# Kernel optimization log

Hardware: AMD Instinct MI355X
Metric: run time of the kernel (lower is better)

Reference implementation:

```python
import jax, jax.numpy as jnp
import numpy as np

D_MODEL = 1024
D_PROJ = D_MODEL // 4


def setup_inputs() -> dict:
    key = jax.random.key(0)
    k1, k2, k3 = jax.random.split(key, 3)
    hidden_states = jax.random.normal(k1, (4, 2048, D_MODEL), dtype=jnp.float32)
    proj_w = jax.random.normal(k2, (D_PROJ, D_MODEL), dtype=jnp.float32) * 0.02
    proj_b = jnp.zeros((D_PROJ,), dtype=jnp.float32)
    clf_w = jax.random.normal(k3, (1, 1), dtype=jnp.float32) * 0.02
    clf_b = jnp.zeros((1,), dtype=jnp.float32)
    return {"hidden_states": hidden_states, "proj_w": proj_w, "proj_b": proj_b,
            "clf_w": clf_w, "clf_b": clf_b}


def reference(hidden_states, proj_w, proj_b, clf_w, clf_b):
    # h: [B, S, D/4]
    h = jax.nn.relu(jnp.einsum('bsd,pd->bsp', hidden_states, proj_w) + proj_b)
    # pairwise dot products == batched h @ h^T: [B, S, S]
    scores = jnp.einsum('bip,bjp->bij', h, h)
    # scalar affine classifier (Linear(1,1)) folded in
    return scores * clf_w[0, 0] + clf_b[0]
```

## Files before the change

kernel.cpp:

```cpp
#include <hip/hip_runtime.h>
#include <hip/hip_bf16.h>

typedef __bf16 bf16_t;
typedef __attribute__((ext_vector_type(8))) __bf16 bf16x8;
typedef __attribute__((ext_vector_type(4))) float f32x4;

#define SEQ    2048
#define DMODEL 1024
#define DPROJ  256
#define NBATCH 4

__device__ __forceinline__ bf16x8 cvt8(const float4& lo, const float4& hi) {
    bf16x8 v;
    v[0] = (bf16_t)lo.x; v[1] = (bf16_t)lo.y; v[2] = (bf16_t)lo.z; v[3] = (bf16_t)lo.w;
    v[4] = (bf16_t)hi.x; v[5] = (bf16_t)hi.y; v[6] = (bf16_t)hi.z; v[7] = (bf16_t)hi.w;
    return v;
}

__device__ __forceinline__ void gl_lds16(const void* g, void* l) {
    __builtin_amdgcn_global_load_lds(
        (const __attribute__((address_space(1))) unsigned int*)g,
        (__attribute__((address_space(3))) unsigned int*)l, 16, 0, 0);
}

__global__ __launch_bounds__(256) void proj_kernel(
    const float* __restrict__ X, const float* __restrict__ W,
    const float* __restrict__ bias, bf16_t* __restrict__ H)
{
    __shared__ __align__(16) bf16_t Xs[64][40];
    __shared__ __align__(16) bf16_t Ws[128][40];

    const int m0 = blockIdx.x * 64;
    const int n0 = blockIdx.y * 128;
    const int tid  = threadIdx.x;
    const int lane = tid & 63;
    const int wave = tid >> 6;
    const int quad = lane >> 4;
    const int l16  = lane & 15;
    const int wm = (wave & 1) * 32;
    const int wn = (wave >> 1) * 64;

    const int xrow = tid >> 2;
    const int xcol = (tid & 3) * 8;
    const int wrow = tid >> 1;
    const int wcol = (tid & 1) * 16;

    f32x4 acc[2][4] = {};

    for (int k0 = 0; k0 < DMODEL; k0 += 32) {
        const float* gx = X + (size_t)(m0 + xrow) * DMODEL + k0 + xcol;
        float4 x0 = *(const float4*)gx;
        float4 x1 = *(const float4*)(gx + 4);
        const float* gw = W + (size_t)(n0 + wrow) * DMODEL + k0 + wcol;
        float4 w0 = *(const float4*)gw;
        float4 w1 = *(const float4*)(gw + 4);
        float4 w2 = *(const float4*)(gw + 8);
        float4 w3 = *(const float4*)(gw + 12);
        __syncthreads();
        *(bf16x8*)&Xs[xrow][xcol]     = cvt8(x0, x1);
        *(bf16x8*)&Ws[wrow][wcol]     = cvt8(w0, w1);
        *(bf16x8*)&Ws[wrow][wcol + 8] = cvt8(w2, w3);
        __syncthreads();

        bf16x8 af[2], bfr[4];
        #pragma unroll
        for (int i = 0; i < 2; ++i)
            af[i] = *(const bf16x8*)&Xs[wm + i * 16 + l16][quad * 8];
        #pragma unroll
        for (int j = 0; j < 4; ++j)
            bfr[j] = *(const bf16x8*)&Ws[wn + j * 16 + l16][quad * 8];
        #pragma unroll
        for (int i = 0; i < 2; ++i)
            #pragma unroll
            for (int j = 0; j < 4; ++j)
                acc[i][j] = __builtin_amdgcn_mfma_f32_16x16x32_bf16(
                    af[i], bfr[j], acc[i][j], 0, 0, 0);
    }

    #pragma unroll
    for (int i = 0; i < 2; ++i) {
        #pragma unroll
        for (int j = 0; j < 4; ++j) {
            const int gn = n0 + wn + j * 16 + l16;
            const float bv = bias[gn];
            #pragma unroll
            for (int r = 0; r < 4; ++r) {
                const int gm = m0 + wm + i * 16 + quad * 4 + r;
                float v = acc[i][j][r] + bv;
                v = v > 0.f ? v : 0.f;
                H[(size_t)gm * DPROJ + gn] = (bf16_t)v;
            }
        }
    }
}

__global__ __launch_bounds__(256) void score_kernel(
    const bf16_t* __restrict__ H, const float* __restrict__ clf_w,
    const float* __restrict__ clf_b, float* __restrict__ Out)
{
    __shared__ __align__(16) bf16_t As[128 * 64];
    __shared__ __align__(16) bf16_t Bs[128 * 64];

    const int b  = blockIdx.z;
    const int m0 = blockIdx.x * 128;
    const int n0 = blockIdx.y * 128;
    const bf16_t* Hb = H + (size_t)b * SEQ * DPROJ;
    float* Ob = Out + (size_t)b * SEQ * SEQ;

    const int tid  = threadIdx.x;
    const int lane = tid & 63;
    const int wave = tid >> 6;
    const int quad = lane >> 4;
    const int l16  = lane & 15;
    const int wm = (wave & 1) * 64;
    const int wn = (wave >> 1) * 64;
    const int swz = l16 & 7;

    const bf16_t* gA[4];
    const bf16_t* gB[4];
    bf16_t* lA[4];
    bf16_t* lB[4];
    #pragma unroll
    for (int t = 0; t < 4; ++t) {
        const int g   = (wave * 4 + t) * 64 + lane;
        const int row = g >> 3;
        const int gc  = (g & 7) ^ (row & 7);
        gA[t] = Hb + (size_t)(m0 + row) * DPROJ + gc * 8;
        gB[t] = Hb + (size_t)(n0 + row) * DPROJ + gc * 8;
        lA[t] = As + (wave * 4 + t) * 512;
        lB[t] = Bs + (wave * 4 + t) * 512;
    }

    f32x4 acc[4][4] = {};

    for (int kt = 0; kt < 4; ++kt) {
        __syncthreads();
        #pragma unroll
        for (int t = 0; t < 4; ++t) {
            gl_lds16(gA[t], lA[t]);
            gl_lds16(gB[t], lB[t]);
        }
        __syncthreads();
        #pragma unroll
        for (int t = 0; t < 4; ++t) { gA[t] += 64; gB[t] += 64; }

        #pragma unroll
        for (int s = 0; s < 2; ++s) {
            const int ch = ((s * 4 + quad) ^ swz) * 8;
            bf16x8 af[4], bfr[4];
            #pragma unroll
            for (int i = 0; i < 4; ++i)
                af[i] = *(const bf16x8*)&As[(wm + i * 16 + l16) * 64 + ch];
            #pragma unroll
            for (int j = 0; j < 4; ++j)
                bfr[j] = *(const bf16x8*)&Bs[(wn + j * 16 + l16) * 64 + ch];
            #pragma unroll
            for (int i = 0; i < 4; ++i)
                #pragma unroll
                for (int j = 0; j < 4; ++j)
                    acc[i][j] = __builtin_amdgcn_mfma_f32_16x16x32_bf16(
                        af[i], bfr[j], acc[i][j], 0, 0, 0);
        }
    }

    const float scale = clf_w[0];
    const float off   = clf_b[0];
    #pragma unroll
    for (int i = 0; i < 4; ++i)
        #pragma unroll
        for (int j = 0; j < 4; ++j)
            #pragma unroll
            for (int r = 0; r < 4; ++r) {
                const int gm = m0 + wm + i * 16 + quad * 4 + r;
                const int gn = n0 + wn + j * 16 + l16;
                Ob[(size_t)gm * SEQ + gn] = acc[i][j][r] * scale + off;
            }
}

extern "C" void kernel_launch(void* const* d_in, const int* in_sizes, int n_in,
                              void* d_out, int out_size, void* d_ws, size_t ws_size,
                              hipStream_t stream) {
    const float* X    = (const float*)d_in[0];
    const float* W    = (const float*)d_in[1];
    const float* bias = (const float*)d_in[2];
    const float* clfw = (const float*)d_in[3];
    const float* clfb = (const float*)d_in[4];
    float* Out = (float*)d_out;
    bf16_t* H  = (bf16_t*)d_ws;

    dim3 g1(NBATCH * SEQ / 64, DPROJ / 128, 1);
    proj_kernel<<<g1, 256, 0, stream>>>(X, W, bias, H);

    dim3 g2(SEQ / 128, SEQ / 128, NBATCH);
    score_kernel<<<g2, 256, 0, stream>>>(H, clfw, clfb, Out);
}
```

Before: 137.6 us.

## Prefetch proj tiles into registers with swizzled LDS; use 8 waves in score kernel

The projection kernel now uses 64x64 tiles with K=64 steps. It prefetches the next K-slab of fp32 X/W into registers while the MFMAs run on the current one, and stores to LDS with an XOR swizzle instead of padding. The score kernel moves from 4 to 8 waves per 128x128 tile, so each wave holds half the accumulators, which gives more waves in flight to hide latency. The costs are extra X reloads in proj (the grid doubles in N) and more LDS readers per tile in the score kernel.

Result: faster. 131.0 us (-4.8%).

```diff
diff --git a/kernel.cpp b/kernel.cpp
--- a/kernel.cpp
+++ b/kernel.cpp
@@ -27,60 +27,90 @@
     const float* __restrict__ X, const float* __restrict__ W,
     const float* __restrict__ bias, bf16_t* __restrict__ H)
 {
-    __shared__ __align__(16) bf16_t Xs[64][40];
-    __shared__ __align__(16) bf16_t Ws[128][40];
+    __shared__ __align__(16) bf16_t Xs[64 * 64];
+    __shared__ __align__(16) bf16_t Ws[64 * 64];
 
     const int m0 = blockIdx.x * 64;
-    const int n0 = blockIdx.y * 128;
+    const int n0 = blockIdx.y * 64;
     const int tid  = threadIdx.x;
     const int lane = tid & 63;
     const int wave = tid >> 6;
     const int quad = lane >> 4;
     const int l16  = lane & 15;
     const int wm = (wave & 1) * 32;
-    const int wn = (wave >> 1) * 64;
-
-    const int xrow = tid >> 2;
-    const int xcol = (tid & 3) * 8;
-    const int wrow = tid >> 1;
-    const int wcol = (tid & 1) * 16;
-
-    f32x4 acc[2][4] = {};
-
-    for (int k0 = 0; k0 < DMODEL; k0 += 32) {
-        const float* gx = X + (size_t)(m0 + xrow) * DMODEL + k0 + xcol;
-        float4 x0 = *(const float4*)gx;
-        float4 x1 = *(const float4*)(gx + 4);
-        const float* gw = W + (size_t)(n0 + wrow) * DMODEL + k0 + wcol;
-        float4 w0 = *(const float4*)gw;
-        float4 w1 = *(const float4*)(gw + 4);
-        float4 w2 = *(const float4*)(gw + 8);
-        float4 w3 = *(const float4*)(gw + 12);
-        __syncthreads();
-        *(bf16x8*)&Xs[xrow][xcol]     = cvt8(x0, x1);
-        *(bf16x8*)&Ws[wrow][wcol]     = cvt8(w0, w1);
-        *(bf16x8*)&Ws[wrow][wcol + 8] = cvt8(w2, w3);
-        __syncthreads();
-
-        bf16x8 af[2], bfr[4];
-        #pragma unroll
-        for (int i = 0; i < 2; ++i)
-            af[i] = *(const bf16x8*)&Xs[wm + i * 16 + l16][quad * 8];
-        #pragma unroll
-        for (int j = 0; j < 4; ++j)
-            bfr[j] = *(const bf16x8*)&Ws[wn + j * 16 + l16][quad * 8];
-        #pragma unroll
-        for (int i = 0; i < 2; ++i)
-            #pragma unroll
-            for (int j = 0; j < 4; ++j)
-                acc[i][j] = __builtin_amdgcn_mfma_f32_16x16x32_bf16(
-                    af[i], bfr[j], acc[i][j], 0, 0, 0);
+    const int wn = (wave >> 1) * 32;
+    const int swz = l16 & 7;
+
+    int srow[2], scol[2];
+    bf16_t* lx[2];
+    bf16_t* lw[2];
+    #pragma unroll
+    for (int r = 0; r < 2; ++r) {
+        const int p = r * 256 + tid;
+        srow[r] = p >> 3;
+        scol[r] = p & 7;
+        const int cs = (scol[r] ^ (srow[r] & 7)) * 8;
+        lx[r] = Xs + srow[r] * 64 + cs;
+        lw[r] = Ws + srow[r] * 64 + cs;
+    }
+
+    float4 xr[2][2], wr[2][2];
+    #pragma unroll
+    for (int r = 0; r < 2; ++r) {
+        const float* gx = X + (size_t)(m0 + srow[r]) * DMODEL + scol[r] * 8;
+        xr[r][0] = *(const float4*)gx;
+        xr[r][1] = *(const float4*)(gx + 4);
+        const float* gw = W + (size_t)(n0 + srow[r]) * DMODEL + scol[r] * 8;
+        wr[r][0] = *(const float4*)gw;
+        wr[r][1] = *(const float4*)(gw + 4);
+    }
+
+    f32x4 acc[2][2] = {};
+
+    for (int kt = 0; kt < 16; ++kt) {
+        __syncthreads();
+        #pragma unroll
+        for (int r = 0; r < 2; ++r) {
+            *(bf16x8*)lx[r] = cvt8(xr[r][0], xr[r][1]);
+            *(bf16x8*)lw[r] = cvt8(wr[r][0], wr[r][1]);
+        }
+        __syncthreads();
+
+        if (kt < 15) {
+            const int k0 = (kt + 1) * 64;
+            #pragma unroll
+            for (int r = 0; r < 2; ++r) {
+                const float* gx = X + (size_t)(m0 + srow[r]) * DMODEL + k0 + scol[r] * 8;
+                xr[r][0] = *(const float4*)gx;
+                xr[r][1] = *(const float4*)(gx + 4);
+                const float* gw = W + (size_t)(n0 + srow[r]) * DMODEL + k0 + scol[r] * 8;
+                wr[r][0] = *(const float4*)gw;
+                wr[r][1] = *(const float4*)(gw + 4);
+            }
+        }
+
+        #pragma unroll
+        for (int ks = 0; ks < 2; ++ks) {
+            bf16x8 af[2], bfr[2];
+            #pragma unroll
+            for (int i = 0; i < 2; ++i) {
+                const int ch = (((ks << 2) | quad) ^ swz) * 8;
+                af[i]  = *(const bf16x8*)&Xs[(wm + i * 16 + l16) * 64 + ch];
+                bfr[i] = *(const bf16x8*)&Ws[(wn + i * 16 + l16) * 64 + ch];
+            }
+            #pragma unroll
+            for (int i = 0; i < 2; ++i)
+                #pragma unroll
+                for (int j = 0; j < 2; ++j)
+                    acc[i][j] = __builtin_amdgcn_mfma_f32_16x16x32_bf16(
+                        af[i], bfr[j], acc[i][j], 0, 0, 0);
+        }
     }
 
     #pragma unroll
     for (int i = 0; i < 2; ++i) {
         #pragma unroll
-        for (int j = 0; j < 4; ++j) {
+        for (int j = 0; j < 2; ++j) {
             const int gn = n0 + wn + j * 16 + l16;
             const float bv = bias[gn];
             #pragma unroll
@@ -94,7 +124,7 @@
     }
 }
 
-__global__ __launch_bounds__(256) void score_kernel(
+__global__ __launch_bounds__(512) void score_kernel(
     const bf16_t* __restrict__ H, const float* __restrict__ clf_w,
     const float* __restrict__ clf_b, float* __restrict__ Out)
 {
@@ -112,50 +142,50 @@
     const int wave = tid >> 6;
     const int quad = lane >> 4;
     const int l16  = lane & 15;
-    const int wm = (wave & 1) * 64;
-    const int wn = (wave >> 1) * 64;
+    const int wm = (wave & 3) * 32;
+    const int wn = (wave >> 2) * 64;
     const int swz = l16 & 7;
 
-    const bf16_t* gA[4];
-    const bf16_t* gB[4];
-    bf16_t* lA[4];
-    bf16_t* lB[4];
-    #pragma unroll
-    for (int t = 0; t < 4; ++t) {
-        const int g   = (wave * 4 + t) * 64 + lane;
+    const bf16_t* gA[2];
+    const bf16_t* gB[2];
+    bf16_t* lA[2];
+    bf16_t* lB[2];
+    #pragma unroll
+    for (int t = 0; t < 2; ++t) {
+        const int g   = (wave * 2 + t) * 64 + lane;
         const int row = g >> 3;
         const int gc  = (g & 7) ^ (row & 7);
         gA[t] = Hb + (size_t)(m0 + row) * DPROJ + gc * 8;
         gB[t] = Hb + (size_t)(n0 + row) * DPROJ + gc * 8;
-        lA[t] = As + (wave * 4 + t) * 512;
-        lB[t] = Bs + (wave * 4 + t) * 512;
-    }
-
-    f32x4 acc[4][4] = {};
+        lA[t] = As + (wave * 2 + t) * 512;
+        lB[t] = Bs + (wave * 2 + t) * 512;
+    }
+
+    f32x4 acc[2][4] = {};
 
     for (int kt = 0; kt < 4; ++kt) {
         __syncthreads();
         #pragma unroll
-        for (int t = 0; t < 4; ++t) {
+        for (int t = 0; t < 2; ++t) {
             gl_lds16(gA[t], lA[t]);
             gl_lds16(gB[t], lB[t]);
         }
         __syncthreads();
         #pragma unroll
-        for (int t = 0; t < 4; ++t) { gA[t] += 64; gB[t] += 64; }
-
-        #pragma unroll
-        for (int s = 0; s < 2; ++s) {
-            const int ch = ((s * 4 + quad) ^ swz) * 8;
-            bf16x8 af[4], bfr[4];
-            #pragma unroll
-            for (int i = 0; i < 4; ++i)
+        for (int t = 0; t < 2; ++t) { gA[t] += 64; gB[t] += 64; }
+
+        #pragma unroll
+        for (int ks = 0; ks < 2; ++ks) {
+            const int ch = (((ks << 2) | quad) ^ swz) * 8;
+            bf16x8 af[2], bfr[4];
+            #pragma unroll
+            for (int i = 0; i < 2; ++i)
                 af[i] = *(const bf16x8*)&As[(wm + i * 16 + l16) * 64 + ch];
             #pragma unroll
             for (int j = 0; j < 4; ++j)
                 bfr[j] = *(const bf16x8*)&Bs[(wn + j * 16 + l16) * 64 + ch];
             #pragma unroll
-            for (int i = 0; i < 4; ++i)
+            for (int i = 0; i < 2; ++i)
                 #pragma unroll
                 for (int j = 0; j < 4; ++j)
                     acc[i][j] = __builtin_amdgcn_mfma_f32_16x16x32_bf16(
@@ -166,7 +196,7 @@
     const float scale = clf_w[0];
     const float off   = clf_b[0];
     #pragma unroll
-    for (int i = 0; i < 4; ++i)
+    for (int i = 0; i < 2; ++i)
         #pragma unroll
         for (int j = 0; j < 4; ++j)
             #pragma unroll
@@ -188,9 +218,9 @@
     float* Out = (float*)d_out;
     bf16_t* H  = (bf16_t*)d_ws;
 
-    dim3 g1(NBATCH * SEQ / 64, DPROJ / 128, 1);
+    dim3 g1(NBATCH * SEQ / 64, DPROJ / 64, 1);
     proj_kernel<<<g1, 256, 0, stream>>>(X, W, bias, H);
 
     dim3 g2(SEQ / 128, SEQ / 128, NBATCH);
-    score_kernel<<<g2, 256, 0, stream>>>(H, clfw, clfb, Out);
-}
+    score_kernel<<<g2, 512, 0, stream>>>(H, clfw, clfb, Out);
+}
```
